# Performance work log

Hardware: AMD Instinct MI355X
Metric: run time of the kernel (lower is better)

Reference implementation:

```python
import jax, jax.numpy as jnp
import numpy as np

TOPK_INC = 20  # top-k vertices per mention that form a hyperedge (torch.topk(attention_a, 20))
TOPK_OUT = 2   # top-k node reps concatenated into the output (torch.topk(X_score, k=2))


def _indicator_from_rows(att, idx):
    # att: [N, N], idx: [A] int. Rows with idx == 0 are skipped, as in the original loop.
    N = att.shape[0]
    rows = att[idx]                                   # [A, N] gather of attention rows
    _, top = jax.lax.top_k(rows, TOPK_INC)            # [A, TOPK_INC]
    mask = (idx != 0).astype(att.dtype)               # [A]
    vals = jnp.broadcast_to(mask[:, None], top.shape).reshape(-1)
    # scatter-max builds the 0/1 incidence vector (multiple mentions OR together)
    return jnp.zeros((N,), att.dtype).at[top.reshape(-1)].max(vals)  # [N]


def _forward_one(h, att, a_idx, b_idx, spk, W_w, W_b, S_w, S_b):
    # h: [N, H], att: [N, N], spk: [N] (single speaker row since speak_num == 1 -> E = 3)
    a_ind = _indicator_from_rows(att, a_idx)
    b_ind = _indicator_from_rows(att, b_idx)
    Hyper0 = jnp.stack([a_ind, b_ind, spk], axis=0)   # [E, N] binary incidence
    Dv = 1.0 / jnp.sqrt(Hyper0.sum(axis=0) + 1.0)     # sqrt(inverse(diag(Dv) + I)) diagonal, [N]
    De = 1.0 / jnp.sqrt(Hyper0.sum(axis=1))           # sqrt(inverse(diag(De))) diagonal, [E]
    Hyper = Hyper0 @ att                              # [E, N]  (dropout is identity in eval)
    Hyper_att = jax.nn.softmax(Hyper, axis=-1)        # F.softmax over last dim for 2D input
    Hyper_prime = Hyper_att @ h                       # [E, H]
    w = jax.nn.softmax(Hyper_prime @ W_w.T + W_b, axis=0)[:, 0]  # [E]
    # A = diag(Dv) @ Hyper0.T @ diag(w) @ diag(De) @ Hyper @ diag(Dv); X = A @ h.
    # Associate as M @ (K @ h) to avoid materializing the [N, N] matrix A.
    K = (w * De)[:, None] * Hyper * Dv[None, :]       # [E, N]
    M = Hyper0.T * Dv[:, None]                        # [N, E]
    X = M @ (K @ h)                                   # [N, H]
    score = (X @ S_w.T + S_b)[:, 0]                   # [N]
    _, top = jax.lax.top_k(score, TOPK_OUT)           # [2]
    return X[top].reshape(-1)                         # [2*H]


def setup_inputs() -> dict:
    key = jax.random.key(0)
    B, N, H, A = 32, 1024, 768, 8
    ks = jax.random.split(key, 8)
    inp = jax.random.normal(ks[0], (B, N, H), dtype=jnp.float32)
    word_att = jax.random.uniform(ks[1], (B, 1, N, N), dtype=jnp.float32)
    a_idx = jax.random.randint(ks[2], (B, A), 0, N)
    b_idx = jax.random.randint(ks[3], (B, A), 0, N)
    speak_num = jnp.ones((B, 1), dtype=jnp.int64 if jax.config.jax_enable_x64 else jnp.int32)
    speak_all = jax.random.randint(ks[4], (B, 3, N), 0, 2).astype(jnp.float32)
    W_w = jax.random.normal(ks[5], (1, H), dtype=jnp.float32) * (1.0 / np.sqrt(H))
    W_b = jnp.zeros((1,), dtype=jnp.float32)
    score_w = jax.random.normal(ks[6], (1, H), dtype=jnp.float32) * (1.0 / np.sqrt(H))
    score_b = jnp.zeros((1,), dtype=jnp.float32)
    return {"input": inp, "word_att": word_att, "a_idx": a_idx, "b_idx": b_idx,
            "speak_num": speak_num, "speak_all": speak_all,
            "W_w": W_w, "W_b": W_b, "score_w": score_w, "score_b": score_b}


def reference(input, word_att, a_idx, b_idx, speak_num, speak_all, W_w, W_b, score_w, score_b):
    # speak_num is all ones by construction -> exactly one speaker hyperedge per sample (E = 3)
    att = word_att[:, 0]           # [B, N, N]
    spk = speak_all[:, 0]          # [B, N]
    f = jax.vmap(_forward_one, in_axes=(0, 0, 0, 0, 0, None, None, None, None))
    return f(input, att, a_idx, b_idx, spk, W_w, W_b, score_w, score_b)  # [B, 2*H]
```

## Files before the change

kernel.cpp:

```cpp
#include <hip/hip_runtime.h>
#include <math.h>

#define B_ 32
#define N_ 1024
#define H_ 768
#define A_ 8
#define TOPK_ 20
#define CH4_ 16

__device__ __forceinline__ float wsum(float x) {
#pragma unroll
    for (int off = 32; off > 0; off >>= 1) x += __shfl_xor(x, off);
    return x;
}

__global__ __launch_bounds__(1024) void k1_ind(
    const float* __restrict__ att, const int* __restrict__ a_idx,
    const int* __restrict__ b_idx, const float* __restrict__ speak_all,
    float* __restrict__ aind, float* __restrict__ bind,
    float* __restrict__ Dv, float* __restrict__ De)
{
    const int b = blockIdx.x;
    const int tid = threadIdx.x;
    const int w = tid >> 6, lane = tid & 63;
    __shared__ float s_ind[2][N_];
    __shared__ float s_red[3][16];

    s_ind[0][tid] = 0.f;
    s_ind[1][tid] = 0.f;
    __syncthreads();

    const int which = w >> 3;
    const int r = w & 7;
    const int idx = which ? b_idx[b * A_ + r] : a_idx[b * A_ + r];
    if (idx != 0) {
        const float* row = att + ((size_t)b * N_ + idx) * N_;
        float v[16];
#pragma unroll
        for (int k = 0; k < 16; ++k) v[k] = row[(k << 6) + lane];
        float* dst = s_ind[which];
        for (int t = 0; t < TOPK_; ++t) {
            float bv = v[0]; int bk = 0;
#pragma unroll
            for (int k = 1; k < 16; ++k)
                if (v[k] > bv) { bv = v[k]; bk = k; }
            int bc = (bk << 6) + lane;
#pragma unroll
            for (int off = 32; off > 0; off >>= 1) {
                float ov = __shfl_xor(bv, off);
                int oc = __shfl_xor(bc, off);
                if (ov > bv || (ov == bv && oc < bc)) { bv = ov; bc = oc; }
            }
            if (lane == 0) dst[bc] = 1.f;
            if (lane == (bc & 63)) v[bc >> 6] = -INFINITY;
        }
    }
    __syncthreads();

    const float sa = s_ind[0][tid], sb = s_ind[1][tid];
    const float ss = speak_all[(size_t)b * 3 * N_ + tid];
    aind[b * N_ + tid] = sa;
    bind[b * N_ + tid] = sb;
    Dv[b * N_ + tid] = 1.f / sqrtf(sa + sb + ss + 1.f);

    float p[3] = {sa, sb, ss};
#pragma unroll
    for (int e = 0; e < 3; ++e) {
        float x = wsum(p[e]);
        if (lane == 0) s_red[e][w] = x;
    }
    __syncthreads();
    if (tid < 3) {
        float s = 0.f;
        for (int i = 0; i < 16; ++i) s += s_red[tid][i];
        De[b * 3 + tid] = 1.f / sqrtf(s);
    }
}

__global__ __launch_bounds__(256) void k2_hyper(
    const float* __restrict__ att, const float* __restrict__ aind,
    const float* __restrict__ bind, const float* __restrict__ speak_all,
    float* __restrict__ Hyper)
{
    const int b = blockIdx.y;
    const int col0 = blockIdx.x * 32;
    const int tid = threadIdx.x;
    const int cx = tid & 7, ry = tid >> 3;
    __shared__ float w0[N_], w1[N_], w2[N_];
    __shared__ float scr[256 * 13];

    for (int n = tid; n < N_; n += 256) {
        w0[n] = aind[b * N_ + n];
        w1[n] = bind[b * N_ + n];
        w2[n] = speak_all[(size_t)b * 3 * N_ + n];
    }
    __syncthreads();

    float a0x=0,a0y=0,a0z=0,a0w=0, a1x=0,a1y=0,a1z=0,a1w=0, a2x=0,a2y=0,a2z=0,a2w=0;
    const float* base = att + (size_t)b * N_ * N_ + col0 + cx * 4;
    for (int n = ry; n < N_; n += 32) {
        const float x0 = w0[n], x1 = w1[n], x2 = w2[n];
        if (x0 == 0.f && x1 == 0.f && x2 == 0.f) continue;
        const float4 v = *(const float4*)(base + (size_t)n * N_);
        a0x += x0*v.x; a0y += x0*v.y; a0z += x0*v.z; a0w += x0*v.w;
        a1x += x1*v.x; a1y += x1*v.y; a1z += x1*v.z; a1w += x1*v.w;
        a2x += x2*v.x; a2y += x2*v.y; a2z += x2*v.z; a2w += x2*v.w;
    }
    __syncthreads();

    float vals[12] = {a0x,a0y,a0z,a0w, a1x,a1y,a1z,a1w, a2x,a2y,a2z,a2w};
#pragma unroll
    for (int k = 0; k < 12; ++k) scr[tid * 13 + k] = vals[k];
    __syncthreads();
    for (int s = 16; s > 0; s >>= 1) {
        if (ry < s) {
#pragma unroll
            for (int k = 0; k < 12; ++k)
                scr[tid * 13 + k] += scr[(tid + s * 8) * 13 + k];
        }
        __syncthreads();
    }
    if (ry == 0) {
#pragma unroll
        for (int e = 0; e < 3; ++e)
#pragma unroll
            for (int j = 0; j < 4; ++j)
                Hyper[(size_t)(b * 3 + e) * N_ + col0 + cx * 4 + j] = scr[tid * 13 + e * 4 + j];
    }
}

__global__ __launch_bounds__(192) void k4_ug(
    const float* __restrict__ h, const float* __restrict__ Hyper,
    const float* __restrict__ Dv, float* __restrict__ UGpart)
{
    const int b = blockIdx.y, c = blockIdx.x;
    const int n0 = c * 64;
    const int t = threadIdx.x;
    const int wv = t >> 6, lane = t & 63;
    __shared__ float sH[3 * N_];
    __shared__ float sw[6][64];
    __shared__ float smz[6];

    for (int i = t; i < 3 * N_; i += 192)
        sH[i] = Hyper[(size_t)b * 3 * N_ + i];
    __syncthreads();

    {
        const float* He = sH + wv * N_;
        float m = -INFINITY;
        for (int n = lane; n < N_; n += 64) m = fmaxf(m, He[n]);
#pragma unroll
        for (int off = 32; off > 0; off >>= 1) m = fmaxf(m, __shfl_xor(m, off));
        float z = 0.f;
        for (int n = lane; n < N_; n += 64) z += expf(He[n] - m);
        z = wsum(z);
        if (lane == 0) { smz[wv] = m; smz[3 + wv] = 1.f / z; }
    }
    __syncthreads();

    {
        const int e = t >> 6, r = t & 63;
        const float Hv = sH[e * N_ + n0 + r];
        sw[e][r] = expf(Hv - smz[e]) * smz[3 + e];
        sw[3 + e][r] = Hv * Dv[b * N_ + n0 + r];
    }
    __syncthreads();

    float u0x=0,u0y=0,u0z=0,u0w=0, u1x=0,u1y=0,u1z=0,u1w=0, u2x=0,u2y=0,u2z=0,u2w=0;
    float g0x=0,g0y=0,g0z=0,g0w=0, g1x=0,g1y=0,g1z=0,g1w=0, g2x=0,g2y=0,g2z=0,g2w=0;
    const float* base = h + (size_t)b * N_ * H_ + (size_t)n0 * H_ + t * 4;
#pragma unroll 8
    for (int r = 0; r < 64; ++r) {
        const float4 v = *(const float4*)(base + (size_t)r * H_);
        const float w0 = sw[0][r], w1 = sw[1][r], w2 = sw[2][r];
        const float g0 = sw[3][r], g1 = sw[4][r], g2 = sw[5][r];
        u0x += w0*v.x; u0y += w0*v.y; u0z += w0*v.z; u0w += w0*v.w;
        u1x += w1*v.x; u1y += w1*v.y; u1z += w1*v.z; u1w += w1*v.w;
        u2x += w2*v.x; u2y += w2*v.y; u2z += w2*v.z; u2w += w2*v.w;
        g0x += g0*v.x; g0y += g0*v.y; g0z += g0*v.z; g0w += g0*v.w;
        g1x += g1*v.x; g1y += g1*v.y; g1z += g1*v.z; g1w += g1*v.w;
        g2x += g2*v.x; g2y += g2*v.y; g2z += g2*v.z; g2w += g2*v.w;
    }
    float* up = UGpart + (size_t)(b * CH4_ + c) * 6 * H_ + t * 4;
    *(float4*)(up)          = make_float4(u0x, u0y, u0z, u0w);
    *(float4*)(up + H_)     = make_float4(u1x, u1y, u1z, u1w);
    *(float4*)(up + 2*H_)   = make_float4(u2x, u2y, u2z, u2w);
    *(float4*)(up + 3*H_)   = make_float4(g0x, g0y, g0z, g0w);
    *(float4*)(up + 4*H_)   = make_float4(g1x, g1y, g1z, g1w);
    *(float4*)(up + 5*H_)   = make_float4(g2x, g2y, g2z, g2w);
}

__global__ __launch_bounds__(256) void k45_fin(
    const float* __restrict__ UGpart,
    const float* __restrict__ De, const float* __restrict__ Dv,
    const float* __restrict__ aind, const float* __restrict__ bind,
    const float* __restrict__ speak_all,
    const float* __restrict__ W_w, const float* __restrict__ W_b,
    const float* __restrict__ S_w, const float* __restrict__ S_b,
    float* __restrict__ out)
{
    const int b = blockIdx.x, tid = threadIdx.x;
    const int lane = tid & 63, wv = tid >> 6;
    __shared__ float sUG[6 * H_];
    __shared__ float sKh[3 * H_];
    __shared__ float sscore[N_];
    __shared__ float sred[16];
    __shared__ int sidx[4];

    {
        const float* p = UGpart + (size_t)b * CH4_ * 6 * H_;
        for (int slot = tid; slot < 1152; slot += 256) {
            const int off = slot * 4;
            float4 a0 = make_float4(0.f, 0.f, 0.f, 0.f);
            float4 a1 = make_float4(0.f, 0.f, 0.f, 0.f);
            for (int c = 0; c < CH4_; c += 2) {
                const float4 v0 = *(const float4*)(p + (size_t)c * 6 * H_ + off);
                const float4 v1 = *(const float4*)(p + (size_t)(c + 1) * 6 * H_ + off);
                a0.x += v0.x; a0.y += v0.y; a0.z += v0.z; a0.w += v0.w;
                a1.x += v1.x; a1.y += v1.y; a1.z += v1.z; a1.w += v1.w;
            }
            sUG[off + 0] = a0.x + a1.x;
            sUG[off + 1] = a0.y + a1.y;
            sUG[off + 2] = a0.z + a1.z;
            sUG[off + 3] = a0.w + a1.w;
        }
    }
    __syncthreads();

    const float* Ub = sUG;
    const float* Gb = sUG + 3 * H_;

    float p0 = 0.f, p1 = 0.f, p2 = 0.f;
    for (int j = tid; j < H_; j += 256) {
        const float ww = W_w[j];
        p0 += Ub[j] * ww; p1 += Ub[H_ + j] * ww; p2 += Ub[2 * H_ + j] * ww;
    }
    p0 = wsum(p0); p1 = wsum(p1); p2 = wsum(p2);
    if (lane == 0) { sred[wv * 3 + 0] = p0; sred[wv * 3 + 1] = p1; sred[wv * 3 + 2] = p2; }
    __syncthreads();
    const float wb = W_b[0];
    const float l0 = sred[0] + sred[3] + sred[6] + sred[9]  + wb;
    const float l1 = sred[1] + sred[4] + sred[7] + sred[10] + wb;
    const float l2 = sred[2] + sred[5] + sred[8] + sred[11] + wb;
    const float mx = fmaxf(l0, fmaxf(l1, l2));
    const float e0 = expf(l0 - mx), e1 = expf(l1 - mx), e2 = expf(l2 - mx);
    const float inv = 1.f / (e0 + e1 + e2);
    const float wd0 = e0 * inv * De[b * 3 + 0];
    const float wd1 = e1 * inv * De[b * 3 + 1];
    const float wd2 = e2 * inv * De[b * 3 + 2];
    __syncthreads();

    for (int j = tid; j < H_; j += 256) {
        sKh[j]          = wd0 * Gb[j];
        sKh[H_ + j]     = wd1 * Gb[H_ + j];
        sKh[2 * H_ + j] = wd2 * Gb[2 * H_ + j];
    }
    __syncthreads();

    float q0 = 0.f, q1 = 0.f, q2 = 0.f;
    for (int j = tid; j < H_; j += 256) {
        const float sw2 = S_w[j];
        q0 += sKh[j] * sw2; q1 += sKh[H_ + j] * sw2; q2 += sKh[2 * H_ + j] * sw2;
    }
    q0 = wsum(q0); q1 = wsum(q1); q2 = wsum(q2);
    if (lane == 0) { sred[wv * 3 + 0] = q0; sred[wv * 3 + 1] = q1; sred[wv * 3 + 2] = q2; }
    __syncthreads();
    q0 = sred[0] + sred[3] + sred[6] + sred[9];
    q1 = sred[1] + sred[4] + sred[7] + sred[10];
    q2 = sred[2] + sred[5] + sred[8] + sred[11];

    const float sb0 = S_b[0];
    const float* av = aind + b * N_;
    const float* bv2 = bind + b * N_;
    const float* dv = Dv + b * N_;
    const float* sv = speak_all + (size_t)b * 3 * N_;
    for (int n = tid; n < N_; n += 256)
        sscore[n] = dv[n] * (av[n] * q0 + bv2[n] * q1 + sv[n] * q2) + sb0;
    __syncthreads();

    int r0;
    {
        float best = -INFINITY; int bi = N_;
        for (int n = tid; n < N_; n += 256) {
            const float s = sscore[n];
            if (s > best || (s == best && n < bi)) { best = s; bi = n; }
        }
#pragma unroll
        for (int off = 32; off > 0; off >>= 1) {
            const float ov = __shfl_xor(best, off); const int oi = __shfl_xor(bi, off);
            if (ov > best || (ov == best && oi < bi)) { best = ov; bi = oi; }
        }
        if (lane == 0) { sred[wv] = best; sidx[wv] = bi; }
        __syncthreads();
        float v = -INFINITY; int i = N_;
        for (int k = 0; k < 4; ++k)
            if (sred[k] > v || (sred[k] == v && sidx[k] < i)) { v = sred[k]; i = sidx[k]; }
        r0 = i;
    }
    __syncthreads();
    int r1;
    {
        float best = -INFINITY; int bi = N_;
        for (int n = tid; n < N_; n += 256) {
            if (n == r0) continue;
            const float s = sscore[n];
            if (s > best || (s == best && n < bi)) { best = s; bi = n; }
        }
#pragma unroll
        for (int off = 32; off > 0; off >>= 1) {
            const float ov = __shfl_xor(best, off); const int oi = __shfl_xor(bi, off);
            if (ov > best || (ov == best && oi < bi)) { best = ov; bi = oi; }
        }
        if (lane == 0) { sred[wv] = best; sidx[wv] = bi; }
        __syncthreads();
        float v = -INFINITY; int i = N_;
        for (int k = 0; k < 4; ++k)
            if (sred[k] > v || (sred[k] == v && sidx[k] < i)) { v = sred[k]; i = sidx[k]; }
        r1 = i;
    }

    float* ob = out + (size_t)b * 2 * H_;
    {
        const float d = dv[r0], wa = av[r0], wbn = bv2[r0], wsv = sv[r0];
        for (int j = tid; j < H_; j += 256)
            ob[j] = d * (wa * sKh[j] + wbn * sKh[H_ + j] + wsv * sKh[2 * H_ + j]);
    }
    {
        const float d = dv[r1], wa = av[r1], wbn = bv2[r1], wsv = sv[r1];
        for (int j = tid; j < H_; j += 256)
            ob[H_ + j] = d * (wa * sKh[j] + wbn * sKh[H_ + j] + wsv * sKh[2 * H_ + j]);
    }
}

extern "C" void kernel_launch(void* const* d_in, const int* in_sizes, int n_in,
                              void* d_out, int out_size, void* d_ws, size_t ws_size,
                              hipStream_t stream)
{
    const float* h         = (const float*)d_in[0];
    const float* att       = (const float*)d_in[1];
    const int*   a_idx     = (const int*)d_in[2];
    const int*   b_idx     = (const int*)d_in[3];
    const float* speak_all = (const float*)d_in[5];
    const float* W_w       = (const float*)d_in[6];
    const float* W_b       = (const float*)d_in[7];
    const float* S_w       = (const float*)d_in[8];
    const float* S_b       = (const float*)d_in[9];
    float* out = (float*)d_out;

    float* ws     = (float*)d_ws;
    float* aind   = ws;
    float* bind   = aind + B_ * N_;
    float* Dv     = bind + B_ * N_;
    float* De     = Dv + B_ * N_;
    float* Hyper  = De + 128;
    float* UGpart = Hyper + B_ * 3 * N_;

    k1_ind<<<B_, 1024, 0, stream>>>(att, a_idx, b_idx, speak_all, aind, bind, Dv, De);
    k2_hyper<<<dim3(32, B_), 256, 0, stream>>>(att, aind, bind, speak_all, Hyper);
    k4_ug<<<dim3(CH4_, B_), 192, 0, stream>>>(h, Hyper, Dv, UGpart);
    k45_fin<<<B_, 256, 0, stream>>>(UGpart, De, Dv, aind, bind, speak_all, W_w, W_b, S_w, S_b, out);
}
```

Before: 83.27 us.

## Compact active rows for hyper matmul, split h pass finer, parallelize partial reduction

k1 now writes a compacted list of active vertices (index plus three incidence weights), padded to a multiple of 256. k2 walks only that list with an 8-deep software-pipelined gather, so it no longer scans all N rows with divergent skips. k4 uses twice as many chunks of 32 rows, with explicit register prefetch, to raise parallelism. The cross-chunk reduction moves out of the per-batch final kernel into a separate grid-wide kernel. This adds one launch, extra workspace and more partial-sum traffic. The speaker row is random 0/1, so about half the rows stay active.

Measured after the change: 82.96 us. About the same (-0.4%).

```diff
diff --git a/kernel.cpp b/kernel.cpp
--- a/kernel.cpp
+++ b/kernel.cpp
@@ -6,7 +6,8 @@
 #define H_ 768
 #define A_ 8
 #define TOPK_ 20
-#define CH4_ 16
+#define CH4_ 32
+#define CMAX_ 1280
 
 __device__ __forceinline__ float wsum(float x) {
 #pragma unroll
@@ -18,13 +19,16 @@
     const float* __restrict__ att, const int* __restrict__ a_idx,
     const int* __restrict__ b_idx, const float* __restrict__ speak_all,
     float* __restrict__ aind, float* __restrict__ bind,
-    float* __restrict__ Dv, float* __restrict__ De)
+    float* __restrict__ Dv, float* __restrict__ De,
+    float4* __restrict__ comp, int* __restrict__ npadArr)
 {
     const int b = blockIdx.x;
     const int tid = threadIdx.x;
     const int w = tid >> 6, lane = tid & 63;
     __shared__ float s_ind[2][N_];
     __shared__ float s_red[3][16];
+    __shared__ int wcnt[16];
+    __shared__ int woff[17];
 
     s_ind[0][tid] = 0.f;
     s_ind[1][tid] = 0.f;
@@ -69,80 +73,120 @@
         float x = wsum(p[e]);
         if (lane == 0) s_red[e][w] = x;
     }
-    __syncthreads();
+
+    const bool act = (sa + sb + ss) > 0.f;
+    const unsigned long long m = __ballot(act);
+    const int wrank = (int)__popcll(m & ((1ull << lane) - 1ull));
+    if (lane == 0) wcnt[w] = (int)__popcll(m);
+    __syncthreads();
+    if (tid == 0) {
+        int s = 0;
+        for (int i = 0; i < 16; ++i) { woff[i] = s; s += wcnt[i]; }
+        woff[16] = s;
+        npadArr[b] = (s + 255) & ~255;
+    }
     if (tid < 3) {
         float s = 0.f;
         for (int i = 0; i < 16; ++i) s += s_red[tid][i];
         De[b * 3 + tid] = 1.f / sqrtf(s);
     }
-}
-
-__global__ __launch_bounds__(256) void k2_hyper(
-    const float* __restrict__ att, const float* __restrict__ aind,
-    const float* __restrict__ bind, const float* __restrict__ speak_all,
-    float* __restrict__ Hyper)
+    __syncthreads();
+    const int nact = woff[16];
+    const int npad = (nact + 255) & ~255;
+    if (act)
+        comp[(size_t)b * CMAX_ + woff[w] + wrank] = make_float4(__int_as_float(tid), sa, sb, ss);
+    for (int i = nact + tid; i < npad; i += 1024)
+        comp[(size_t)b * CMAX_ + i] = make_float4(__int_as_float(0), 0.f, 0.f, 0.f);
+}
+
+__global__ __launch_bounds__(256, 2) void k2_hyper(
+    const float* __restrict__ att, const float4* __restrict__ comp,
+    const int* __restrict__ npadArr, float* __restrict__ Hyper)
 {
     const int b = blockIdx.y;
     const int col0 = blockIdx.x * 32;
-    const int tid = threadIdx.x;
-    const int cx = tid & 7, ry = tid >> 3;
-    __shared__ float w0[N_], w1[N_], w2[N_];
+    const int t = threadIdx.x;
+    const int cx = t & 7, ig = t >> 3;
+    __shared__ float4 scomp[1024];
     __shared__ float scr[256 * 13];
 
-    for (int n = tid; n < N_; n += 256) {
-        w0[n] = aind[b * N_ + n];
-        w1[n] = bind[b * N_ + n];
-        w2[n] = speak_all[(size_t)b * 3 * N_ + n];
-    }
+    const int npad = npadArr[b];
+    for (int i = t; i < npad; i += 256) scomp[i] = comp[(size_t)b * CMAX_ + i];
     __syncthreads();
 
     float a0x=0,a0y=0,a0z=0,a0w=0, a1x=0,a1y=0,a1z=0,a1w=0, a2x=0,a2y=0,a2z=0,a2w=0;
-    const float* base = att + (size_t)b * N_ * N_ + col0 + cx * 4;
-    for (int n = ry; n < N_; n += 32) {
-        const float x0 = w0[n], x1 = w1[n], x2 = w2[n];
-        if (x0 == 0.f && x1 == 0.f && x2 == 0.f) continue;
-        const float4 v = *(const float4*)(base + (size_t)n * N_);
-        a0x += x0*v.x; a0y += x0*v.y; a0z += x0*v.z; a0w += x0*v.w;
-        a1x += x1*v.x; a1y += x1*v.y; a1z += x1*v.z; a1w += x1*v.w;
-        a2x += x2*v.x; a2y += x2*v.y; a2z += x2*v.z; a2w += x2*v.w;
+    const float* bb = att + (size_t)b * N_ * N_ + col0 + cx * 4;
+
+    if (npad > 0) {
+        float4 v[8], cw[8];
+        int i = ig;
+#pragma unroll
+        for (int k = 0; k < 8; ++k) {
+            const float4 c = scomp[i];
+            cw[k] = c;
+            v[k] = *(const float4*)(bb + (size_t)__float_as_int(c.x) * N_);
+            i += 32;
+        }
+        while (i < npad) {
+#pragma unroll
+            for (int k = 0; k < 8; ++k) {
+                const float4 cur = v[k];
+                const float4 cc = cw[k];
+                const float4 nc = scomp[i];
+                cw[k] = nc;
+                v[k] = *(const float4*)(bb + (size_t)__float_as_int(nc.x) * N_);
+                a0x += cc.y*cur.x; a0y += cc.y*cur.y; a0z += cc.y*cur.z; a0w += cc.y*cur.w;
+                a1x += cc.z*cur.x; a1y += cc.z*cur.y; a1z += cc.z*cur.z; a1w += cc.z*cur.w;
+                a2x += cc.w*cur.x; a2y += cc.w*cur.y; a2z += cc.w*cur.z; a2w += cc.w*cur.w;
+                i += 32;
+            }
+        }
+#pragma unroll
+        for (int k = 0; k < 8; ++k) {
+            const float4 cur = v[k];
+            const float4 cc = cw[k];
+            a0x += cc.y*cur.x; a0y += cc.y*cur.y; a0z += cc.y*cur.z; a0w += cc.y*cur.w;
+            a1x += cc.z*cur.x; a1y += cc.z*cur.y; a1z += cc.z*cur.z; a1w += cc.z*cur.w;
+            a2x += cc.w*cur.x; a2y += cc.w*cur.y; a2z += cc.w*cur.z; a2w += cc.w*cur.w;
+        }
     }
     __syncthreads();
 
     float vals[12] = {a0x,a0y,a0z,a0w, a1x,a1y,a1z,a1w, a2x,a2y,a2z,a2w};
 #pragma unroll
-    for (int k = 0; k < 12; ++k) scr[tid * 13 + k] = vals[k];
+    for (int k = 0; k < 12; ++k) scr[t * 13 + k] = vals[k];
     __syncthreads();
     for (int s = 16; s > 0; s >>= 1) {
-        if (ry < s) {
+        if (ig < s) {
 #pragma unroll
             for (int k = 0; k < 12; ++k)
-                scr[tid * 13 + k] += scr[(tid + s * 8) * 13 + k];
+                scr[t * 13 + k] += scr[(t + s * 8) * 13 + k];
         }
         __syncthreads();
     }
-    if (ry == 0) {
+    if (ig == 0) {
 #pragma unroll
         for (int e = 0; e < 3; ++e)
 #pragma unroll
             for (int j = 0; j < 4; ++j)
-                Hyper[(size_t)(b * 3 + e) * N_ + col0 + cx * 4 + j] = scr[tid * 13 + e * 4 + j];
-    }
-}
-
-__global__ __launch_bounds__(192) void k4_ug(
+                Hyper[(size_t)(b * 3 + e) * N_ + col0 + cx * 4 + j] = scr[t * 13 + e * 4 + j];
+    }
+}
+
+__global__ __launch_bounds__(192, 2) void k4_ug(
     const float* __restrict__ h, const float* __restrict__ Hyper,
     const float* __restrict__ Dv, float* __restrict__ UGpart)
 {
     const int b = blockIdx.y, c = blockIdx.x;
-    const int n0 = c * 64;
+    const int n0 = c * 32;
     const int t = threadIdx.x;
     const int wv = t >> 6, lane = t & 63;
     __shared__ float sH[3 * N_];
-    __shared__ float sw[6][64];
+    __shared__ float sw6[6][32];
     __shared__ float smz[6];
 
-    for (int i = t; i < 3 * N_; i += 192)
-        sH[i] = Hyper[(size_t)b * 3 * N_ + i];
+    for (int i = t; i < 3 * N_ / 4; i += 192)
+        ((float4*)sH)[i] = ((const float4*)(Hyper + (size_t)b * 3 * N_))[i];
     __syncthreads();
 
     {
@@ -157,29 +201,37 @@
         if (lane == 0) { smz[wv] = m; smz[3 + wv] = 1.f / z; }
     }
     __syncthreads();
-
-    {
-        const int e = t >> 6, r = t & 63;
+    if (t < 96) {
+        const int e = t >> 5, r = t & 31;
         const float Hv = sH[e * N_ + n0 + r];
-        sw[e][r] = expf(Hv - smz[e]) * smz[3 + e];
-        sw[3 + e][r] = Hv * Dv[b * N_ + n0 + r];
+        sw6[e][r] = expf(Hv - smz[e]) * smz[3 + e];
+        sw6[3 + e][r] = Hv * Dv[b * N_ + n0 + r];
     }
     __syncthreads();
 
     float u0x=0,u0y=0,u0z=0,u0w=0, u1x=0,u1y=0,u1z=0,u1w=0, u2x=0,u2y=0,u2z=0,u2w=0;
     float g0x=0,g0y=0,g0z=0,g0w=0, g1x=0,g1y=0,g1z=0,g1w=0, g2x=0,g2y=0,g2z=0,g2w=0;
     const float* base = h + (size_t)b * N_ * H_ + (size_t)n0 * H_ + t * 4;
-#pragma unroll 8
-    for (int r = 0; r < 64; ++r) {
-        const float4 v = *(const float4*)(base + (size_t)r * H_);
-        const float w0 = sw[0][r], w1 = sw[1][r], w2 = sw[2][r];
-        const float g0 = sw[3][r], g1 = sw[4][r], g2 = sw[5][r];
-        u0x += w0*v.x; u0y += w0*v.y; u0z += w0*v.z; u0w += w0*v.w;
-        u1x += w1*v.x; u1y += w1*v.y; u1z += w1*v.z; u1w += w1*v.w;
-        u2x += w2*v.x; u2y += w2*v.y; u2z += w2*v.z; u2w += w2*v.w;
-        g0x += g0*v.x; g0y += g0*v.y; g0z += g0*v.z; g0w += g0*v.w;
-        g1x += g1*v.x; g1y += g1*v.y; g1z += g1*v.z; g1w += g1*v.w;
-        g2x += g2*v.x; g2y += g2*v.y; g2z += g2*v.z; g2w += g2*v.w;
+
+    float4 v[8];
+#pragma unroll
+    for (int k = 0; k < 8; ++k) v[k] = *(const float4*)(base + (size_t)k * H_);
+#pragma unroll
+    for (int r8 = 0; r8 < 32; r8 += 8) {
+#pragma unroll
+        for (int k = 0; k < 8; ++k) {
+            const int r = r8 + k;
+            const float4 cur = v[k];
+            if (r + 8 < 32) v[k] = *(const float4*)(base + (size_t)(r + 8) * H_);
+            const float w0 = sw6[0][r], w1 = sw6[1][r], w2 = sw6[2][r];
+            const float g0 = sw6[3][r], g1 = sw6[4][r], g2 = sw6[5][r];
+            u0x += w0*cur.x; u0y += w0*cur.y; u0z += w0*cur.z; u0w += w0*cur.w;
+            u1x += w1*cur.x; u1y += w1*cur.y; u1z += w1*cur.z; u1w += w1*cur.w;
+            u2x += w2*cur.x; u2y += w2*cur.y; u2z += w2*cur.z; u2w += w2*cur.w;
+            g0x += g0*cur.x; g0y += g0*cur.y; g0z += g0*cur.z; g0w += g0*cur.w;
+            g1x += g1*cur.x; g1y += g1*cur.y; g1z += g1*cur.z; g1w += g1*cur.w;
+            g2x += g2*cur.x; g2y += g2*cur.y; g2z += g2*cur.z; g2w += g2*cur.w;
+        }
     }
     float* up = UGpart + (size_t)(b * CH4_ + c) * 6 * H_ + t * 4;
     *(float4*)(up)          = make_float4(u0x, u0y, u0z, u0w);
@@ -190,8 +242,37 @@
     *(float4*)(up + 5*H_)   = make_float4(g2x, g2y, g2z, g2w);
 }
 
-__global__ __launch_bounds__(256) void k45_fin(
-    const float* __restrict__ UGpart,
+__global__ __launch_bounds__(256, 2) void k4b_red(
+    const float* __restrict__ UGpart, float* __restrict__ U, float* __restrict__ G)
+{
+    const int gid = blockIdx.x * 256 + threadIdx.x;
+    const int b = gid / 1152;
+    const int rem = gid % 1152;
+    const int s = rem / 192;
+    const int col = (rem % 192) * 4;
+
+    const float* p = UGpart + (size_t)b * CH4_ * 6 * H_ + s * H_ + col;
+    float4 a0 = make_float4(0,0,0,0), a1 = make_float4(0,0,0,0);
+    float4 a2 = make_float4(0,0,0,0), a3 = make_float4(0,0,0,0);
+#pragma unroll
+    for (int c = 0; c < CH4_; c += 4) {
+        const float4 v0 = *(const float4*)(p + (size_t)(c + 0) * 6 * H_);
+        const float4 v1 = *(const float4*)(p + (size_t)(c + 1) * 6 * H_);
+        const float4 v2 = *(const float4*)(p + (size_t)(c + 2) * 6 * H_);
+        const float4 v3 = *(const float4*)(p + (size_t)(c + 3) * 6 * H_);
+        a0.x += v0.x; a0.y += v0.y; a0.z += v0.z; a0.w += v0.w;
+        a1.x += v1.x; a1.y += v1.y; a1.z += v1.z; a1.w += v1.w;
+        a2.x += v2.x; a2.y += v2.y; a2.z += v2.z; a2.w += v2.w;
+        a3.x += v3.x; a3.y += v3.y; a3.z += v3.z; a3.w += v3.w;
+    }
+    const float4 acc = make_float4(a0.x+a1.x+a2.x+a3.x, a0.y+a1.y+a2.y+a3.y,
+                                   a0.z+a1.z+a2.z+a3.z, a0.w+a1.w+a2.w+a3.w);
+    if (s < 3) *(float4*)(U + ((size_t)(b * 3 + s)) * H_ + col) = acc;
+    else       *(float4*)(G + ((size_t)(b * 3 + s - 3)) * H_ + col) = acc;
+}
+
+__global__ __launch_bounds__(256) void k5_fin(
+    const float* __restrict__ U, const float* __restrict__ G,
     const float* __restrict__ De, const float* __restrict__ Dv,
     const float* __restrict__ aind, const float* __restrict__ bind,
     const float* __restrict__ speak_all,
@@ -201,34 +282,13 @@
 {
     const int b = blockIdx.x, tid = threadIdx.x;
     const int lane = tid & 63, wv = tid >> 6;
-    __shared__ float sUG[6 * H_];
     __shared__ float sKh[3 * H_];
     __shared__ float sscore[N_];
     __shared__ float sred[16];
     __shared__ int sidx[4];
 
-    {
-        const float* p = UGpart + (size_t)b * CH4_ * 6 * H_;
-        for (int slot = tid; slot < 1152; slot += 256) {
-            const int off = slot * 4;
-            float4 a0 = make_float4(0.f, 0.f, 0.f, 0.f);
-            float4 a1 = make_float4(0.f, 0.f, 0.f, 0.f);
-            for (int c = 0; c < CH4_; c += 2) {
-                const float4 v0 = *(const float4*)(p + (size_t)c * 6 * H_ + off);
-                const float4 v1 = *(const float4*)(p + (size_t)(c + 1) * 6 * H_ + off);
-                a0.x += v0.x; a0.y += v0.y; a0.z += v0.z; a0.w += v0.w;
-                a1.x += v1.x; a1.y += v1.y; a1.z += v1.z; a1.w += v1.w;
-            }
-            sUG[off + 0] = a0.x + a1.x;
-            sUG[off + 1] = a0.y + a1.y;
-            sUG[off + 2] = a0.z + a1.z;
-            sUG[off + 3] = a0.w + a1.w;
-        }
-    }
-    __syncthreads();
-
-    const float* Ub = sUG;
-    const float* Gb = sUG + 3 * H_;
+    const float* Ub = U + (size_t)b * 3 * H_;
+    const float* Gb = G + (size_t)b * 3 * H_;
 
     float p0 = 0.f, p1 = 0.f, p2 = 0.f;
     for (int j = tid; j < H_; j += 256) {
@@ -347,16 +407,21 @@
     const float* S_b       = (const float*)d_in[9];
     float* out = (float*)d_out;
 
-    float* ws     = (float*)d_ws;
-    float* aind   = ws;
-    float* bind   = aind + B_ * N_;
-    float* Dv     = bind + B_ * N_;
-    float* De     = Dv + B_ * N_;
-    float* Hyper  = De + 128;
-    float* UGpart = Hyper + B_ * 3 * N_;
-
-    k1_ind<<<B_, 1024, 0, stream>>>(att, a_idx, b_idx, speak_all, aind, bind, Dv, De);
-    k2_hyper<<<dim3(32, B_), 256, 0, stream>>>(att, aind, bind, speak_all, Hyper);
+    float* ws      = (float*)d_ws;
+    float* aind    = ws;
+    float* bind    = aind + B_ * N_;
+    float* Dv      = bind + B_ * N_;
+    float* De      = Dv + B_ * N_;
+    int*   npadArr = (int*)(De + 128);
+    float4* comp   = (float4*)(De + 256);
+    float* Hyper   = De + 256 + B_ * CMAX_ * 4;
+    float* UGpart  = Hyper + B_ * 3 * N_;
+    float* U       = UGpart + (size_t)B_ * CH4_ * 6 * H_;
+    float* G       = U + B_ * 3 * H_;
+
+    k1_ind<<<B_, 1024, 0, stream>>>(att, a_idx, b_idx, speak_all, aind, bind, Dv, De, comp, npadArr);
+    k2_hyper<<<dim3(32, B_), 256, 0, stream>>>(att, comp, npadArr, Hyper);
     k4_ug<<<dim3(CH4_, B_), 192, 0, stream>>>(h, Hyper, Dv, UGpart);
-    k45_fin<<<B_, 256, 0, stream>>>(UGpart, De, Dv, aind, bind, speak_all, W_w, W_b, S_w, S_b, out);
-}
+    k4b_red<<<144, 256, 0, stream>>>(UGpart, U, G);
+    k5_fin<<<B_, 256, 0, stream>>>(U, G, De, Dv, aind, bind, speak_all, W_w, W_b, S_w, S_b, out);
+}
```
